# Optimization experiments

Measured on AMD Instinct MI355X. Metric: run time of the kernel, lower is better.

## Reference

```python
import jax, jax.numpy as jnp
import numpy as np

E = 1024
B = 16384

def _ln(x, g, b, eps=1e-5):
    mu = jnp.mean(x, axis=-1, keepdims=True)
    var = jnp.mean(jnp.square(x - mu), axis=-1, keepdims=True)
    return (x - mu) * jax.lax.rsqrt(var + eps) * g + b

def setup_inputs() -> dict:
    key = jax.random.key(0)
    ks = jax.random.split(key, 16)
    s = 0.02
    return {
        'img_feat': jax.random.normal(ks[0], (B, E), jnp.float32),
        'txt_feat': jax.random.normal(ks[1], (B, E), jnp.float32),
        # MHA 1 (img queries txt): packed in_proj [3E, E] like torch
        'w_in1': jax.random.normal(ks[2], (3 * E, E), jnp.float32) * s,
        'b_in1': jnp.zeros((3 * E,), jnp.float32),
        'w_out1': jax.random.normal(ks[3], (E, E), jnp.float32) * s,
        'b_out1': jnp.zeros((E,), jnp.float32),
        # MHA 2 (txt queries img)
        'w_in2': jax.random.normal(ks[4], (3 * E, E), jnp.float32) * s,
        'b_in2': jnp.zeros((3 * E,), jnp.float32),
        'w_out2': jax.random.normal(ks[5], (E, E), jnp.float32) * s,
        'b_out2': jnp.zeros((E,), jnp.float32),
        # LayerNorms
        'g1': jnp.ones((E,), jnp.float32), 'be1': jnp.zeros((E,), jnp.float32),
        'g2': jnp.ones((E,), jnp.float32), 'be2': jnp.zeros((E,), jnp.float32),
        'g3': jnp.ones((E,), jnp.float32), 'be3': jnp.zeros((E,), jnp.float32),
        # FFN
        'w_ffn1': jax.random.normal(ks[6], (4 * E, E), jnp.float32) * s,
        'b_ffn1': jnp.zeros((4 * E,), jnp.float32),
        'w_ffn2': jax.random.normal(ks[7], (E, 4 * E), jnp.float32) * s,
        'b_ffn2': jnp.zeros((E,), jnp.float32),
    }

def _attn_seq1(q_in, kv_in, w_in, b_in, w_out, b_out):
    # seq_len==1 for both query and key: softmax over a single 1x1 score is
    # identically 1, so attention output == out_proj(v_proj(kv)). The q/k
    # projections cancel out exactly (same math as torch MHA in eval mode).
    wv = w_in[2 * E:]
    bv = b_in[2 * E:]
    v = kv_in @ wv.T + bv          # [B, E]
    return v @ w_out.T + b_out     # [B, E]

def reference(img_feat, txt_feat, w_in1, b_in1, w_out1, b_out1,
              w_in2, b_in2, w_out2, b_out2,
              g1, be1, g2, be2, g3, be3,
              w_ffn1, b_ffn1, w_ffn2, b_ffn2):
    img_att = _attn_seq1(img_feat, txt_feat, w_in1, b_in1, w_out1, b_out1)
    img = _ln(img_feat + img_att, g1, be1)
    txt_att = _attn_seq1(txt_feat, img, w_in2, b_in2, w_out2, b_out2)
    txt = _ln(txt_feat + txt_att, g2, be2)
    combined = img + txt
    h = jax.nn.gelu(combined @ w_ffn1.T + b_ffn1, approximate=False)
    ffn = h @ w_ffn2.T + b_ffn2
    return _ln(combined + ffn, g3, be3)
```

## Files before the change

kernel.cpp:

```cpp
#include <hip/hip_runtime.h>
#include <hip/hip_bf16.h>

typedef __bf16 bf16_t;
typedef __bf16 bf16x8 __attribute__((ext_vector_type(8)));
typedef __bf16 bf16x4 __attribute__((ext_vector_type(4)));
typedef float f32x4 __attribute__((ext_vector_type(4)));

static constexpr int E = 1024;
static constexpr int BROWS = 16384;
static constexpr size_t MB = 1ull << 20;

__device__ __forceinline__ float gelu_f(float x) {
  float t = __expf(-x * fmaf(0.0713548163f, x * x, 1.5957691216f));
  return x / (1.0f + t);
}

__global__ __launch_bounds__(256) void cvt_f32_bf16(const float* __restrict__ src,
                                                    bf16_t* __restrict__ dst, int n4) {
  int stride = gridDim.x * blockDim.x;
  for (int i = blockIdx.x * blockDim.x + threadIdx.x; i < n4; i += stride) {
    float4 v = reinterpret_cast<const float4*>(src)[i];
    bf16x4 o;
    o[0] = (bf16_t)v.x; o[1] = (bf16_t)v.y; o[2] = (bf16_t)v.z; o[3] = (bf16_t)v.w;
    reinterpret_cast<bf16x4*>(dst)[i] = o;
  }
}

__global__ __launch_bounds__(256) void cvt_transpose(const float* __restrict__ in,
                                                     bf16_t* __restrict__ out) {
  __shared__ float t[64][65];
  const int bx = blockIdx.x * 64, by = blockIdx.y * 64;
  const int tid = threadIdx.x;
  const int r = tid >> 2, c4 = (tid & 3) * 16;
#pragma unroll
  for (int j = 0; j < 4; ++j) {
    float4 v = *reinterpret_cast<const float4*>(&in[(long)(by + r) * E + bx + c4 + j * 4]);
    t[r][c4 + j * 4 + 0] = v.x;
    t[r][c4 + j * 4 + 1] = v.y;
    t[r][c4 + j * 4 + 2] = v.z;
    t[r][c4 + j * 4 + 3] = v.w;
  }
  __syncthreads();
#pragma unroll
  for (int j = 0; j < 16; j += 4) {
    bf16x4 o;
    o[0] = (bf16_t)t[c4 + j + 0][r];
    o[1] = (bf16_t)t[c4 + j + 1][r];
    o[2] = (bf16_t)t[c4 + j + 2][r];
    o[3] = (bf16_t)t[c4 + j + 3][r];
    *reinterpret_cast<bf16x4*>(&out[(long)(bx + r) * E + by + c4 + j]) = o;
  }
}

__global__ __launch_bounds__(256) void fuse_bias(const float* __restrict__ wo,
                                                 const float* __restrict__ bv,
                                                 const float* __restrict__ bo,
                                                 float* __restrict__ outb) {
  const int row = (blockIdx.x * 256 + threadIdx.x) >> 6;
  const int lane = threadIdx.x & 63;
  float s = 0.f;
  for (int k = lane; k < E; k += 64) s += wo[(long)row * E + k] * bv[k];
#pragma unroll
  for (int off = 32; off; off >>= 1) s += __shfl_down(s, off);
  if (lane == 0) outb[row] = s + bo[row];
}

__global__ __launch_bounds__(256) void gemm_bt_small(const bf16_t* __restrict__ A,
                                                     const bf16_t* __restrict__ Bw,
                                                     bf16_t* __restrict__ Cout, int K, int N,
                                                     int NBX) {
  const int nwg = gridDim.x;
  const int orig = blockIdx.x;
  const int q = nwg >> 3;
  const int wgid = (orig & 7) * q + (orig >> 3);
  const int bx = wgid % NBX;
  const int by = wgid / NBX;
  __shared__ bf16_t As[128 * 32];
  __shared__ bf16_t Bs[128 * 32];
  const int tid = threadIdx.x;
  const int lane = tid & 63;
  const int w = tid >> 6;
  const int wr = w >> 1, wc = w & 1;
  const long m0 = (long)by * 128;
  const long n0 = (long)bx * 128;
  const bf16_t* aSrc = A + (m0 + (tid >> 2)) * (long)K + (tid & 3) * 8;
  const bf16_t* bSrc = Bw + (n0 + (tid >> 2)) * (long)K + (tid & 3) * 8;
  f32x4 acc[4][4];
#pragma unroll
  for (int mi = 0; mi < 4; ++mi)
#pragma unroll
    for (int ni = 0; ni < 4; ++ni) acc[mi][ni] = {0.f, 0.f, 0.f, 0.f};
  const int nkt = K >> 5;
  for (int kt = 0; kt < nkt; ++kt) {
#pragma unroll
    for (int r = 0; r < 2; ++r) {
      __builtin_amdgcn_global_load_lds(
          (__attribute__((address_space(1))) void*)(aSrc + (long)r * 64 * K + kt * 32),
          (__attribute__((address_space(3))) void*)((char*)As + r * 4096 + w * 1024), 16, 0, 0);
      __builtin_amdgcn_global_load_lds(
          (__attribute__((address_space(1))) void*)(bSrc + (long)r * 64 * K + kt * 32),
          (__attribute__((address_space(3))) void*)((char*)Bs + r * 4096 + w * 1024), 16, 0, 0);
    }
    __syncthreads();
    bf16x8 af[4], bfv[4];
#pragma unroll
    for (int i = 0; i < 4; ++i) {
      af[i] = *reinterpret_cast<const bf16x8*>(
          &As[(wr * 64 + i * 16 + (lane & 15)) * 32 + (lane >> 4) * 8]);
      bfv[i] = *reinterpret_cast<const bf16x8*>(
          &Bs[(wc * 64 + i * 16 + (lane & 15)) * 32 + (lane >> 4) * 8]);
    }
#pragma unroll
    for (int mi = 0; mi < 4; ++mi)
#pragma unroll
      for (int ni = 0; ni < 4; ++ni)
        acc[mi][ni] = __builtin_amdgcn_mfma_f32_16x16x32_bf16(af[mi], bfv[ni], acc[mi][ni], 0, 0, 0);
    __syncthreads();
  }
  const long crow0 = m0 + wr * 64 + ((lane >> 4) * 4);
  const long ccol0 = n0 + wc * 64 + (lane & 15);
#pragma unroll
  for (int mi = 0; mi < 4; ++mi)
#pragma unroll
    for (int ni = 0; ni < 4; ++ni)
#pragma unroll
      for (int r = 0; r < 4; ++r)
        Cout[(crow0 + mi * 16 + r) * N + ccol0 + ni * 16] = (bf16_t)acc[mi][ni][r];
}

#define GLDS(gp, lp)                                                              \
  __builtin_amdgcn_global_load_lds((__attribute__((address_space(1))) void*)(gp), \
                                   (__attribute__((address_space(3))) void*)(lp), 16, 0, 0)

template <int ACT_GELU, int OUT_BF16>
__global__ __launch_bounds__(512) void gemm256(const bf16_t* __restrict__ A,
                                               const bf16_t* __restrict__ Bw,
                                               const float* __restrict__ bias,
                                               void* __restrict__ Cout, int K, int N, int NBX) {
  __shared__ char smem[131072];
  const int nwg = gridDim.x;
  const int orig = blockIdx.x;
  const int q = nwg >> 3;
  const int wgid = (orig & 7) * q + (orig >> 3);
  const int bx = wgid % NBX;
  const int by = wgid / NBX;
  const long m0 = (long)by * 256;
  const long n0 = (long)bx * 256;

  const int tid = threadIdx.x;
  const int lane = tid & 63;
  const int w = tid >> 6;
  const int wr = w >> 2;
  const int wc = w & 3;

  const int sv = (lane & 7) ^ (lane >> 3);
  const int r2 = (lane >> 3) * 2 + (sv >> 2);
  const int kc = (sv & 3) * 8;
  const bf16_t* srcA0 = A + (m0 + w * 32 + r2) * (long)K + kc;
  const bf16_t* srcA1 = srcA0 + 16 * (long)K;
  const bf16_t* srcB0 = Bw + (n0 + w * 32 + r2) * (long)K + kc;
  const bf16_t* srcB1 = srcB0 + 16 * (long)K;

#define STAGE_A(s, t)                                                   \
  {                                                                     \
    GLDS(srcA0 + (long)(t) * 32, smem + (s) * 32768 + w * 2048);        \
    GLDS(srcA1 + (long)(t) * 32, smem + (s) * 32768 + w * 2048 + 1024); \
  }
#define STAGE_B(s, t)                                                           \
  {                                                                             \
    GLDS(srcB0 + (long)(t) * 32, smem + (s) * 32768 + 16384 + w * 2048);        \
    GLDS(srcB1 + (long)(t) * 32, smem + (s) * 32768 + 16384 + w * 2048 + 1024); \
  }

  const int laneoff =
      ((lane >> 1) & 7) * 128 +
      ((((((lane & 1) << 2) | (lane >> 4))) ^ ((lane >> 1) & 7)) << 4);
  const int wrOff = wr * 8192;
  const int wcOff = wc * 4096;

  f32x4 acc[8][4];
#pragma unroll
  for (int mi = 0; mi < 8; ++mi)
#pragma unroll
    for (int ni = 0; ni < 4; ++ni) acc[mi][ni] = {0.f, 0.f, 0.f, 0.f};

  STAGE_A(0, 0); STAGE_B(0, 0);
  STAGE_A(1, 1); STAGE_B(1, 1);
  STAGE_A(2, 2); STAGE_B(2, 2);
  asm volatile("s_waitcnt vmcnt(8)" ::: "memory");
  asm volatile("s_barrier" ::: "memory");

  const int NS = K >> 5;
#pragma unroll 1
  for (int j = 0; j < NS; ++j) {
    const int slot = j & 3;
    const char* sb = smem + slot * 32768;

    if (j + 3 < NS) STAGE_A((j + 3) & 3, j + 3);
    bf16x8 a[8], b[4];
#pragma unroll
    for (int i = 0; i < 8; ++i)
      a[i] = *reinterpret_cast<const bf16x8*>(sb + wrOff + i * 1024 + laneoff);
#pragma unroll
    for (int i = 0; i < 4; ++i)
      b[i] = *reinterpret_cast<const bf16x8*>(sb + 16384 + wcOff + i * 1024 + laneoff);
    if (j + 3 < NS) STAGE_B((j + 3) & 3, j + 3);

    asm volatile("s_barrier" ::: "memory");
    __builtin_amdgcn_sched_barrier(0);

    __builtin_amdgcn_s_setprio(1);
#pragma unroll
    for (int mi = 0; mi < 8; ++mi)
#pragma unroll
      for (int ni = 0; ni < 4; ++ni)
        acc[mi][ni] = __builtin_amdgcn_mfma_f32_16x16x32_bf16(a[mi], b[ni], acc[mi][ni], 0, 0, 0);
    __builtin_amdgcn_s_setprio(0);

    if (j + 1 < NS) {
      if (j <= NS - 4)
        asm volatile("s_waitcnt vmcnt(8)" ::: "memory");
      else if (j == NS - 3)
        asm volatile("s_waitcnt vmcnt(4)" ::: "memory");
      else
        asm volatile("s_waitcnt vmcnt(0)" ::: "memory");
    }
    asm volatile("s_barrier" ::: "memory");
  }

  float bv[4];
#pragma unroll
  for (int ni = 0; ni < 4; ++ni) bv[ni] = bias[n0 + wc * 64 + ni * 16 + (lane & 15)];
  const long crow0 = m0 + wr * 128 + ((lane >> 4) * 4);
  const long ccol0 = n0 + wc * 64 + (lane & 15);
#pragma unroll
  for (int mi = 0; mi < 8; ++mi) {
#pragma unroll
    for (int ni = 0; ni < 4; ++ni) {
#pragma unroll
      for (int rr = 0; rr < 4; ++rr) {
        float v = acc[mi][ni][rr] + bv[ni];
        if (ACT_GELU) v = gelu_f(v);
        long idx = (crow0 + mi * 16 + rr) * N + ccol0 + ni * 16;
        if (OUT_BF16)
          ((bf16_t*)Cout)[idx] = (bf16_t)v;
        else
          ((float*)Cout)[idx] = v;
      }
    }
  }
}
#undef STAGE_A
#undef STAGE_B
#undef GLDS

template <int MODE>
__global__ __launch_bounds__(256) void ln_k(const float* __restrict__ Xf,
                                            const bf16_t* __restrict__ Xb,
                                            const float* __restrict__ Yf,
                                            const bf16_t* __restrict__ Yb,
                                            const float* __restrict__ gamma,
                                            const float* __restrict__ beta,
                                            const bf16_t* __restrict__ addB,
                                            float* __restrict__ outF,
                                            bf16_t* __restrict__ outB) {
  const int tid = threadIdx.x;
  const long base = (long)blockIdx.x * E;
  float4 s;
  if (MODE < 2) {
    float4 xv = reinterpret_cast<const float4*>(Xf + base)[tid];
    bf16x4 yv = reinterpret_cast<const bf16x4*>(Yb + base)[tid];
    s.x = xv.x + (float)yv[0]; s.y = xv.y + (float)yv[1];
    s.z = xv.z + (float)yv[2]; s.w = xv.w + (float)yv[3];
  } else {
    bf16x4 xv = reinterpret_cast<const bf16x4*>(Xb + base)[tid];
    float4 yv = reinterpret_cast<const float4*>(Yf + base)[tid];
    s.x = (float)xv[0] + yv.x; s.y = (float)xv[1] + yv.y;
    s.z = (float)xv[2] + yv.z; s.w = (float)xv[3] + yv.w;
  }
  float sum = s.x + s.y + s.z + s.w;
  float sq = s.x * s.x + s.y * s.y + s.z * s.z + s.w * s.w;
#pragma unroll
  for (int off = 32; off > 0; off >>= 1) {
    sum += __shfl_down(sum, off);
    sq += __shfl_down(sq, off);
  }
  __shared__ float red[2][4];
  const int w = tid >> 6;
  if ((tid & 63) == 0) { red[0][w] = sum; red[1][w] = sq; }
  __syncthreads();
  float tot = red[0][0] + red[0][1] + red[0][2] + red[0][3];
  float tsq = red[1][0] + red[1][1] + red[1][2] + red[1][3];
  const float mu = tot * (1.0f / E);
  const float var = tsq * (1.0f / E) - mu * mu;
  const float rs = rsqrtf(var + 1e-5f);
  float4 gv = reinterpret_cast<const float4*>(gamma)[tid];
  float4 bvv = reinterpret_cast<const float4*>(beta)[tid];
  float4 o;
  o.x = (s.x - mu) * rs * gv.x + bvv.x;
  o.y = (s.y - mu) * rs * gv.y + bvv.y;
  o.z = (s.z - mu) * rs * gv.z + bvv.z;
  o.w = (s.w - mu) * rs * gv.w + bvv.w;
  if (MODE == 1) {
    bf16x4 av = reinterpret_cast<const bf16x4*>(addB + base)[tid];
    o.x += (float)av[0]; o.y += (float)av[1]; o.z += (float)av[2]; o.w += (float)av[3];
  }
  if (MODE == 2) {
    reinterpret_cast<float4*>(outF + base)[tid] = o;
  } else {
    bf16x4 ob;
    ob[0] = (bf16_t)o.x; ob[1] = (bf16_t)o.y; ob[2] = (bf16_t)o.z; ob[3] = (bf16_t)o.w;
    reinterpret_cast<bf16x4*>(outB + base)[tid] = ob;
  }
}

extern "C" void kernel_launch(void* const* d_in, const int* in_sizes, int n_in, void* d_out,
                              int out_size, void* d_ws, size_t ws_size, hipStream_t stream) {
  const float* img_feat = (const float*)d_in[0];
  const float* txt_feat = (const float*)d_in[1];
  const float* w_in1 = (const float*)d_in[2];
  const float* b_in1 = (const float*)d_in[3];
  const float* w_out1 = (const float*)d_in[4];
  const float* b_out1 = (const float*)d_in[5];
  const float* w_in2 = (const float*)d_in[6];
  const float* b_in2 = (const float*)d_in[7];
  const float* w_out2 = (const float*)d_in[8];
  const float* b_out2 = (const float*)d_in[9];
  const float* g1 = (const float*)d_in[10];
  const float* be1 = (const float*)d_in[11];
  const float* g2 = (const float*)d_in[12];
  const float* be2 = (const float*)d_in[13];
  const float* g3 = (const float*)d_in[14];
  const float* be3 = (const float*)d_in[15];
  const float* w_ffn1 = (const float*)d_in[16];
  const float* b_ffn1 = (const float*)d_in[17];
  const float* w_ffn2 = (const float*)d_in[18];
  const float* b_ffn2 = (const float*)d_in[19];

  if (ws_size < 184 * MB) return;
  char* ws = (char*)d_ws;
  bf16_t* TXTB = (bf16_t*)(ws + 0 * MB);
  bf16_t* ATT = (bf16_t*)(ws + 32 * MB);
  bf16_t* IMGB = (bf16_t*)(ws + 64 * MB);
  bf16_t* H = (bf16_t*)(ws + 0 * MB);
  bf16_t* COMB = (bf16_t*)(ws + 128 * MB);
  bf16_t* T0 = (bf16_t*)(ws + 160 * MB);
  bf16_t* T1 = (bf16_t*)(ws + 162 * MB);
  bf16_t* Wc1 = (bf16_t*)(ws + 164 * MB);
  bf16_t* Wc2 = (bf16_t*)(ws + 166 * MB);
  bf16_t* wf1b = (bf16_t*)(ws + 168 * MB);
  bf16_t* wf2b = (bf16_t*)(ws + 176 * MB);
  float* bias1 = (float*)d_out;
  float* bias2 = bias1 + E;

  dim3 blk(256);
  dim3 blk512(512);
  cvt_f32_bf16<<<dim3(2048), blk, 0, stream>>>(txt_feat, TXTB, BROWS * E / 4);
  cvt_f32_bf16<<<dim3(1024), blk, 0, stream>>>(w_ffn1, wf1b, 4 * E * E / 4);
  cvt_f32_bf16<<<dim3(1024), blk, 0, stream>>>(w_ffn2, wf2b, 4 * E * E / 4);

  cvt_transpose<<<dim3(16, 16), blk, 0, stream>>>(w_in1 + 2 * E * E, T0);
  cvt_f32_bf16<<<dim3(512), blk, 0, stream>>>(w_out1, T1, E * E / 4);
  gemm_bt_small<<<dim3(64), blk, 0, stream>>>(T1, T0, Wc1, E, E, 8);
  fuse_bias<<<dim3(256), blk, 0, stream>>>(w_out1, b_in1 + 2 * E, b_out1, bias1);

  cvt_transpose<<<dim3(16, 16), blk, 0, stream>>>(w_in2 + 2 * E * E, T0);
  cvt_f32_bf16<<<dim3(512), blk, 0, stream>>>(w_out2, T1, E * E / 4);
  gemm_bt_small<<<dim3(64), blk, 0, stream>>>(T1, T0, Wc2, E, E, 8);
  fuse_bias<<<dim3(256), blk, 0, stream>>>(w_out2, b_in2 + 2 * E, b_out2, bias2);

  gemm256<0, 1><<<dim3(256), blk512, 0, stream>>>(TXTB, Wc1, bias1, ATT, E, E, 4);
  ln_k<0><<<dim3(BROWS), blk, 0, stream>>>(img_feat, nullptr, nullptr, ATT, g1, be1, nullptr,
                                           nullptr, IMGB);
  gemm256<0, 1><<<dim3(256), blk512, 0, stream>>>(IMGB, Wc2, bias2, ATT, E, E, 4);
  ln_k<1><<<dim3(BROWS), blk, 0, stream>>>(txt_feat, nullptr, nullptr, ATT, g2, be2, IMGB,
                                           nullptr, COMB);
  gemm256<1, 1><<<dim3(1024), blk512, 0, stream>>>(COMB, wf1b, b_ffn1, H, E, 4 * E, 16);
  gemm256<0, 0><<<dim3(256), blk512, 0, stream>>>(H, wf2b, b_ffn2, d_out, 4 * E, E, 4);
  ln_k<2><<<dim3(BROWS), blk, 0, stream>>>(nullptr, COMB, (float*)d_out, nullptr, g3, be3,
                                           nullptr, (float*)d_out, nullptr);
}
```

Baseline: 555.1 us.

## Double-buffer GEMM LDS fragments in registers to overlap reads with MFMA

Restructures the GEMM main loop so the next K-step's A/B fragments are read from LDS into a second register set while the MFMAs for the current step run. The loop is unrolled by two, ping-ponging between the two register buffers. One barrier per iteration is dropped, and the vmcnt waits are retuned because both global-to-LDS stages are now issued together. This is meant to hide LDS read latency behind matrix math and cut synchronisation. The cost is roughly 96 extra VGPRs for the second fragment set, which risks lower occupancy or spills.

```diff
diff --git a/kernel.cpp b/kernel.cpp
--- a/kernel.cpp
+++ b/kernel.cpp
@@ -178,6 +178,32 @@
   const int wrOff = wr * 8192;
   const int wcOff = wc * 4096;
 
+#define RDFRAG(sidx, ar, br)                                                          \
+  {                                                                                   \
+    const char* sbp = smem + (sidx) * 32768;                                          \
+    _Pragma("unroll") for (int i = 0; i < 8; ++i) ar[i] =                             \
+        *reinterpret_cast<const bf16x8*>(sbp + wrOff + i * 1024 + laneoff);           \
+    _Pragma("unroll") for (int i = 0; i < 4; ++i) br[i] =                             \
+        *reinterpret_cast<const bf16x8*>(sbp + 16384 + wcOff + i * 1024 + laneoff);   \
+  }
+
+#define ITER(j, ca, cb, na, nb)                                                        \
+  {                                                                                    \
+    if ((j) + 3 < NS) { STAGE_A(((j) + 3) & 3, (j) + 3); STAGE_B(((j) + 3) & 3, (j) + 3); } \
+    if ((j) + 1 < NS) RDFRAG(((j) + 1) & 3, na, nb);                                   \
+    __builtin_amdgcn_s_setprio(1);                                                     \
+    _Pragma("unroll") for (int mi = 0; mi < 8; ++mi)                                   \
+        _Pragma("unroll") for (int ni = 0; ni < 4; ++ni) acc[mi][ni] =                 \
+            __builtin_amdgcn_mfma_f32_16x16x32_bf16(ca[mi], cb[ni], acc[mi][ni], 0, 0, 0); \
+    __builtin_amdgcn_s_setprio(0);                                                     \
+    asm volatile("s_waitcnt lgkmcnt(0)" ::: "memory");                                 \
+    if ((j) <= NS - 4)                                                                 \
+      asm volatile("s_waitcnt vmcnt(4)" ::: "memory");                                 \
+    else if ((j) == NS - 3)                                                            \
+      asm volatile("s_waitcnt vmcnt(0)" ::: "memory");                                 \
+    asm volatile("s_barrier" ::: "memory");                                            \
+  }
+
   f32x4 acc[8][4];
 #pragma unroll
   for (int mi = 0; mi < 8; ++mi)
@@ -187,45 +213,16 @@
   STAGE_A(0, 0); STAGE_B(0, 0);
   STAGE_A(1, 1); STAGE_B(1, 1);
   STAGE_A(2, 2); STAGE_B(2, 2);
-  asm volatile("s_waitcnt vmcnt(8)" ::: "memory");
+  asm volatile("s_waitcnt vmcnt(4)" ::: "memory");
   asm volatile("s_barrier" ::: "memory");
 
   const int NS = K >> 5;
+  bf16x8 aA[8], bA[4], aB[8], bB[4];
+  RDFRAG(0, aA, bA);
 #pragma unroll 1
-  for (int j = 0; j < NS; ++j) {
-    const int slot = j & 3;
-    const char* sb = smem + slot * 32768;
-
-    if (j + 3 < NS) STAGE_A((j + 3) & 3, j + 3);
-    bf16x8 a[8], b[4];
-#pragma unroll
-    for (int i = 0; i < 8; ++i)
-      a[i] = *reinterpret_cast<const bf16x8*>(sb + wrOff + i * 1024 + laneoff);
-#pragma unroll
-    for (int i = 0; i < 4; ++i)
-      b[i] = *reinterpret_cast<const bf16x8*>(sb + 16384 + wcOff + i * 1024 + laneoff);
-    if (j + 3 < NS) STAGE_B((j + 3) & 3, j + 3);
-
-    asm volatile("s_barrier" ::: "memory");
-    __builtin_amdgcn_sched_barrier(0);
-
-    __builtin_amdgcn_s_setprio(1);
-#pragma unroll
-    for (int mi = 0; mi < 8; ++mi)
-#pragma unroll
-      for (int ni = 0; ni < 4; ++ni)
-        acc[mi][ni] = __builtin_amdgcn_mfma_f32_16x16x32_bf16(a[mi], b[ni], acc[mi][ni], 0, 0, 0);
-    __builtin_amdgcn_s_setprio(0);
-
-    if (j + 1 < NS) {
-      if (j <= NS - 4)
-        asm volatile("s_waitcnt vmcnt(8)" ::: "memory");
-      else if (j == NS - 3)
-        asm volatile("s_waitcnt vmcnt(4)" ::: "memory");
-      else
-        asm volatile("s_waitcnt vmcnt(0)" ::: "memory");
-    }
-    asm volatile("s_barrier" ::: "memory");
+  for (int j = 0; j < NS; j += 2) {
+    ITER(j, aA, bA, aB, bB);
+    ITER(j + 1, aB, bB, aA, bA);
   }
 
   float bv[4];
@@ -249,9 +246,11 @@
       }
     }
   }
-}
+#undef ITER
+#undef RDFRAG
 #undef STAGE_A
 #undef STAGE_B
+}
 #undef GLDS
 
 template <int MODE>
```

New measurement: 552.3 us. No clear change (-0.5%).

## Shrink GEMM tile to 128x256 with double buffering for higher occupancy

Applied to the files above, without the earlier changes.

Replaces the 256x256-tile, 4-stage pipelined GEMM with a 128x256 tile that uses a 2-stage double buffer and 48KB of LDS. It also requests 4 waves per SIMD via launch bounds and doubles the grid sizes. The goal is more concurrent workgroups per CU, better load balance across CUs, and latency hiding through occupancy rather than deep prefetch. The cost is lower arithmetic intensity per tile, more redundant B-tile loads, and a full vmcnt(0) wait plus barrier every K-step, which shortens the software pipeline.

```diff
diff --git a/kernel.cpp b/kernel.cpp
--- a/kernel.cpp
+++ b/kernel.cpp
@@ -133,18 +133,19 @@
                                    (__attribute__((address_space(3))) void*)(lp), 16, 0, 0)
 
 template <int ACT_GELU, int OUT_BF16>
-__global__ __launch_bounds__(512) void gemm256(const bf16_t* __restrict__ A,
-                                               const bf16_t* __restrict__ Bw,
-                                               const float* __restrict__ bias,
-                                               void* __restrict__ Cout, int K, int N, int NBX) {
-  __shared__ char smem[131072];
+__global__ __launch_bounds__(512, 4) void gemm128(const bf16_t* __restrict__ A,
+                                                  const bf16_t* __restrict__ Bw,
+                                                  const float* __restrict__ bias,
+                                                  void* __restrict__ Cout, int K, int N,
+                                                  int NBX) {
+  __shared__ char smem[49152];
   const int nwg = gridDim.x;
   const int orig = blockIdx.x;
   const int q = nwg >> 3;
   const int wgid = (orig & 7) * q + (orig >> 3);
   const int bx = wgid % NBX;
   const int by = wgid / NBX;
-  const long m0 = (long)by * 256;
+  const long m0 = (long)by * 128;
   const long n0 = (long)bx * 256;
 
   const int tid = threadIdx.x;
@@ -156,85 +157,65 @@
   const int sv = (lane & 7) ^ (lane >> 3);
   const int r2 = (lane >> 3) * 2 + (sv >> 2);
   const int kc = (sv & 3) * 8;
-  const bf16_t* srcA0 = A + (m0 + w * 32 + r2) * (long)K + kc;
-  const bf16_t* srcA1 = srcA0 + 16 * (long)K;
+  const bf16_t* srcA = A + (m0 + w * 16 + r2) * (long)K + kc;
   const bf16_t* srcB0 = Bw + (n0 + w * 32 + r2) * (long)K + kc;
   const bf16_t* srcB1 = srcB0 + 16 * (long)K;
-
-#define STAGE_A(s, t)                                                   \
-  {                                                                     \
-    GLDS(srcA0 + (long)(t) * 32, smem + (s) * 32768 + w * 2048);        \
-    GLDS(srcA1 + (long)(t) * 32, smem + (s) * 32768 + w * 2048 + 1024); \
-  }
-#define STAGE_B(s, t)                                                           \
-  {                                                                             \
-    GLDS(srcB0 + (long)(t) * 32, smem + (s) * 32768 + 16384 + w * 2048);        \
-    GLDS(srcB1 + (long)(t) * 32, smem + (s) * 32768 + 16384 + w * 2048 + 1024); \
-  }
 
   const int laneoff =
       ((lane >> 1) & 7) * 128 +
       ((((((lane & 1) << 2) | (lane >> 4))) ^ ((lane >> 1) & 7)) << 4);
-  const int wrOff = wr * 8192;
+  const int wrOff = wr * 4096;
   const int wcOff = wc * 4096;
 
-  f32x4 acc[8][4];
-#pragma unroll
-  for (int mi = 0; mi < 8; ++mi)
+  f32x4 acc[4][4];
+#pragma unroll
+  for (int mi = 0; mi < 4; ++mi)
 #pragma unroll
     for (int ni = 0; ni < 4; ++ni) acc[mi][ni] = {0.f, 0.f, 0.f, 0.f};
 
-  STAGE_A(0, 0); STAGE_B(0, 0);
-  STAGE_A(1, 1); STAGE_B(1, 1);
-  STAGE_A(2, 2); STAGE_B(2, 2);
-  asm volatile("s_waitcnt vmcnt(8)" ::: "memory");
+  GLDS(srcA, smem + w * 1024);
+  GLDS(srcB0, smem + 8192 + w * 2048);
+  GLDS(srcB1, smem + 8192 + w * 2048 + 1024);
+  asm volatile("s_waitcnt vmcnt(0)" ::: "memory");
   asm volatile("s_barrier" ::: "memory");
 
   const int NS = K >> 5;
 #pragma unroll 1
   for (int j = 0; j < NS; ++j) {
-    const int slot = j & 3;
-    const char* sb = smem + slot * 32768;
-
-    if (j + 3 < NS) STAGE_A((j + 3) & 3, j + 3);
-    bf16x8 a[8], b[4];
-#pragma unroll
-    for (int i = 0; i < 8; ++i)
+    const char* sb = smem + (j & 1) * 24576;
+    if (j + 1 < NS) {
+      char* sd = smem + ((j + 1) & 1) * 24576;
+      const long t = (long)(j + 1) * 32;
+      GLDS(srcA + t, sd + w * 1024);
+      GLDS(srcB0 + t, sd + 8192 + w * 2048);
+      GLDS(srcB1 + t, sd + 8192 + w * 2048 + 1024);
+    }
+    bf16x8 a[4], b[4];
+#pragma unroll
+    for (int i = 0; i < 4; ++i)
       a[i] = *reinterpret_cast<const bf16x8*>(sb + wrOff + i * 1024 + laneoff);
 #pragma unroll
     for (int i = 0; i < 4; ++i)
-      b[i] = *reinterpret_cast<const bf16x8*>(sb + 16384 + wcOff + i * 1024 + laneoff);
-    if (j + 3 < NS) STAGE_B((j + 3) & 3, j + 3);
-
-    asm volatile("s_barrier" ::: "memory");
-    __builtin_amdgcn_sched_barrier(0);
-
+      b[i] = *reinterpret_cast<const bf16x8*>(sb + 8192 + wcOff + i * 1024 + laneoff);
     __builtin_amdgcn_s_setprio(1);
 #pragma unroll
-    for (int mi = 0; mi < 8; ++mi)
+    for (int mi = 0; mi < 4; ++mi)
 #pragma unroll
       for (int ni = 0; ni < 4; ++ni)
         acc[mi][ni] = __builtin_amdgcn_mfma_f32_16x16x32_bf16(a[mi], b[ni], acc[mi][ni], 0, 0, 0);
     __builtin_amdgcn_s_setprio(0);
-
-    if (j + 1 < NS) {
-      if (j <= NS - 4)
-        asm volatile("s_waitcnt vmcnt(8)" ::: "memory");
-      else if (j == NS - 3)
-        asm volatile("s_waitcnt vmcnt(4)" ::: "memory");
-      else
-        asm volatile("s_waitcnt vmcnt(0)" ::: "memory");
-    }
+    asm volatile("s_waitcnt lgkmcnt(0)" ::: "memory");
+    if (j + 1 < NS) asm volatile("s_waitcnt vmcnt(0)" ::: "memory");
     asm volatile("s_barrier" ::: "memory");
   }
 
   float bv[4];
 #pragma unroll
   for (int ni = 0; ni < 4; ++ni) bv[ni] = bias[n0 + wc * 64 + ni * 16 + (lane & 15)];
-  const long crow0 = m0 + wr * 128 + ((lane >> 4) * 4);
+  const long crow0 = m0 + wr * 64 + ((lane >> 4) * 4);
   const long ccol0 = n0 + wc * 64 + (lane & 15);
 #pragma unroll
-  for (int mi = 0; mi < 8; ++mi) {
+  for (int mi = 0; mi < 4; ++mi) {
 #pragma unroll
     for (int ni = 0; ni < 4; ++ni) {
 #pragma unroll
@@ -250,8 +231,6 @@
     }
   }
 }
-#undef STAGE_A
-#undef STAGE_B
 #undef GLDS
 
 template <int MODE>
@@ -369,14 +348,14 @@
   gemm_bt_small<<<dim3(64), blk, 0, stream>>>(T1, T0, Wc2, E, E, 8);
   fuse_bias<<<dim3(256), blk, 0, stream>>>(w_out2, b_in2 + 2 * E, b_out2, bias2);
 
-  gemm256<0, 1><<<dim3(256), blk512, 0, stream>>>(TXTB, Wc1, bias1, ATT, E, E, 4);
+  gemm128<0, 1><<<dim3(512), blk512, 0, stream>>>(TXTB, Wc1, bias1, ATT, E, E, 4);
   ln_k<0><<<dim3(BROWS), blk, 0, stream>>>(img_feat, nullptr, nullptr, ATT, g1, be1, nullptr,
                                            nullptr, IMGB);
-  gemm256<0, 1><<<dim3(256), blk512, 0, stream>>>(IMGB, Wc2, bias2, ATT, E, E, 4);
+  gemm128<0, 1><<<dim3(512), blk512, 0, stream>>>(IMGB, Wc2, bias2, ATT, E, E, 4);
   ln_k<1><<<dim3(BROWS), blk, 0, stream>>>(txt_feat, nullptr, nullptr, ATT, g2, be2, IMGB,
                                            nullptr, COMB);
-  gemm256<1, 1><<<dim3(1024), blk512, 0, stream>>>(COMB, wf1b, b_ffn1, H, E, 4 * E, 16);
-  gemm256<0, 0><<<dim3(256), blk512, 0, stream>>>(H, wf2b, b_ffn2, d_out, 4 * E, E, 4);
+  gemm128<1, 1><<<dim3(2048), blk512, 0, stream>>>(COMB, wf1b, b_ffn1, H, E, 4 * E, 16);
+  gemm128<0, 0><<<dim3(512), blk512, 0, stream>>>(H, wf2b, b_ffn2, d_out, 4 * E, E, 4);
   ln_k<2><<<dim3(BROWS), blk, 0, stream>>>(nullptr, COMB, (float*)d_out, nullptr, g3, be3,
                                            nullptr, (float*)d_out, nullptr);
 }
```

Measured after the change: 568.1 us. 1.02x slower.
